# Performance work log

Measured on AMD Instinct MI355X. Metric: run time of the kernel, lower is better.

Reference implementation:

```python
import jax, jax.numpy as jnp
import numpy as np

EMBED_DIM = 1024
NUM_HEADS = 16
MICRO_HEADS = 8
HEAD_DIM = EMBED_DIM // NUM_HEADS
N_BLOCKS = NUM_HEADS // MICRO_HEADS
B, N = 2, 2048


def setup_inputs() -> dict:
    key = jax.random.key(0)
    ks = jax.random.split(key, 9)
    s = 1.0 / np.sqrt(EMBED_DIM)
    return {
        "x": jax.random.normal(ks[0], (B, N, EMBED_DIM), dtype=jnp.float32),
        "Wq": jax.random.uniform(ks[1], (EMBED_DIM, EMBED_DIM), jnp.float32, -s, s),
        "bq": jax.random.uniform(ks[2], (EMBED_DIM,), jnp.float32, -s, s),
        "Wk": jax.random.uniform(ks[3], (EMBED_DIM, EMBED_DIM), jnp.float32, -s, s),
        "bk": jax.random.uniform(ks[4], (EMBED_DIM,), jnp.float32, -s, s),
        "Wv": jax.random.uniform(ks[5], (EMBED_DIM, EMBED_DIM), jnp.float32, -s, s),
        "bv": jax.random.uniform(ks[6], (EMBED_DIM,), jnp.float32, -s, s),
        "Wo": jax.random.uniform(ks[7], (EMBED_DIM, EMBED_DIM), jnp.float32, -s, s),
        "bo": jax.random.uniform(ks[8], (EMBED_DIM,), jnp.float32, -s, s),
    }


def _scramble(t, b, n):
    # Replicates torch's Qh[:, :, hs:he, :].contiguous().view(B*mh, N, dh)
    # which is a raw row-major reshape mixing (N, mh) -> (mh, N) per batch.
    # (B, N, E) -> (B, N, nb, mh, dh) -> (B, nb, N, mh, dh) -> raw reshape -> (B, nb, mh, N, dh)
    t = t.reshape(b, n, N_BLOCKS, MICRO_HEADS, HEAD_DIM)
    t = jnp.transpose(t, (0, 2, 1, 3, 4))
    return t.reshape(b, N_BLOCKS, MICRO_HEADS, n, HEAD_DIM)


def reference(x, Wq, bq, Wk, bk, Wv, bv, Wo, bo):
    b, n, e = x.shape
    scale = HEAD_DIM ** -0.5
    Q = x @ Wq.T + bq
    K = x @ Wk.T + bk
    V = x @ Wv.T + bv
    q = _scramble(Q, b, n)  # (B, nb, mh, N, dh)
    k = _scramble(K, b, n)
    v = _scramble(V, b, n)
    s = jnp.einsum("bgmqd,bgmkd->bgmqk", q, k) * scale  # (B, nb, mh, N, N)
    causal = jnp.tril(jnp.ones((n, n), dtype=bool))
    s = jnp.where(causal, s, -jnp.inf)
    p = jax.nn.softmax(s, axis=-1)
    ctx = jnp.einsum("bgmqk,bgmkd->bgmqd", p, v)  # (B, nb, mh, N, dh)
    # inverse raw reshape: (mh, N, dh) -> (N, mh*dh) per (b, g), then concat blocks
    ctx = ctx.reshape(b, N_BLOCKS, n, MICRO_HEADS * HEAD_DIM)
    ctx = jnp.transpose(ctx, (0, 2, 1, 3)).reshape(b, n, e)
    return ctx @ Wo.T + bo
```

## Files before the change

### kernel.cpp

```cpp
#include <hip/hip_runtime.h>
#include <hip/hip_bf16.h>


typedef unsigned short ushortT;
typedef __attribute__((ext_vector_type(8))) short short8;
typedef __attribute__((ext_vector_type(4))) float floatx4;

__device__ inline float bf2f(ushortT u) {
    union { unsigned int i; float f; } v; v.i = ((unsigned int)u) << 16; return v.f;
}
__device__ inline ushortT f2bf(float f) {
    union { float f; unsigned int i; } v; v.f = f;
    unsigned int x = v.i;
    return (ushortT)((x + 0x7fffu + ((x >> 16) & 1u)) >> 16);
}

__device__ inline void gl_lds16(const ushortT* g, ushortT* lds) {
    __builtin_amdgcn_global_load_lds(
        (const __attribute__((address_space(1))) unsigned int*)g,
        (__attribute__((address_space(3))) unsigned int*)lds, 16, 0, 0);
}

__global__ __launch_bounds__(256) void cvt_bf16(
    const float* __restrict__ x,
    const float* __restrict__ Wq, const float* __restrict__ Wk,
    const float* __restrict__ Wv, const float* __restrict__ Wo,
    ushortT* __restrict__ xb, ushortT* __restrict__ Wb)
{
    const unsigned tid = blockIdx.x * 256 + threadIdx.x;
    const size_t e = (size_t)tid * 8;
    const float* src;
    ushortT* dst;
    size_t off;
    if (e < (size_t)(4u << 20)) { src = x; dst = xb; off = e; }
    else {
        const size_t r = e - (size_t)(4u << 20);
        const int wsel = (int)(r >> 20);
        off = r & 0xFFFFFu;
        src = (wsel == 0) ? Wq : (wsel == 1) ? Wk : (wsel == 2) ? Wv : Wo;
        dst = Wb + ((size_t)wsel << 20);
    }
    const float4 f0 = ((const float4*)(src + off))[0];
    const float4 f1 = ((const float4*)(src + off))[1];
    union { __hip_bfloat162 h[4]; uint4 u; } pk;
    pk.h[0] = __float22bfloat162_rn(float2{f0.x, f0.y});
    pk.h[1] = __float22bfloat162_rn(float2{f0.z, f0.w});
    pk.h[2] = __float22bfloat162_rn(float2{f1.x, f1.y});
    pk.h[3] = __float22bfloat162_rn(float2{f1.z, f1.w});
    *(uint4*)(dst + off) = pk.u;
}

__global__ __launch_bounds__(512, 2) void gemm_qkv_8p(
    const ushortT* __restrict__ A, const ushortT* __restrict__ Wst,
    const float* __restrict__ b0, const float* __restrict__ b1, const float* __restrict__ b2,
    ushortT* __restrict__ O0, ushortT* __restrict__ O1, ushortT* __restrict__ O2)
{
    __shared__ __align__(16) ushortT sm[65536];

    const int t = threadIdx.x;
    const int bid = blockIdx.x;
    const int wg = (bid & 7) * 24 + (bid >> 3);
    const int mt = wg / 12;
    const int nt = wg - mt * 12;
    const int m0 = mt * 256;
    const int mat = nt >> 2;
    const int n0 = (nt & 3) * 256;
    const ushortT* W = Wst + ((size_t)mat << 20);
    const float* bias = (mat == 0) ? b0 : (mat == 1) ? b1 : b2;
    ushortT* Out     = (mat == 0) ? O0 : (mat == 1) ? O1 : O2;

    const int w = t >> 6, lane = t & 63;
    const int wm = w >> 2, wn = w & 3;
    const int col16 = lane & 15, quad = lane >> 4;
    const int c7 = col16 & 7;

    const int ko[2] = { ((0 + quad) ^ c7) << 3, ((4 + quad) ^ c7) << 3 };
    const int xbase = (wm * 128 + col16) * 64;
    const int wbase = (wn * 64 + col16) * 64;

    const int trow = t >> 3;
    const int sch = (t & 7) ^ (trow & 7);
    const ushortT* gA[4]; const ushortT* gB[4];
    #pragma unroll
    for (int q = 0; q < 4; q++) {
        gA[q] = A + (size_t)(m0 + q * 64 + trow) * 1024 + sch * 8;
        gB[q] = W + (size_t)(n0 + q * 64 + trow) * 1024 + sch * 8;
    }
    const int dst0 = (w << 6) * 8;

    floatx4 acc[8][4];
    #pragma unroll
    for (int i = 0; i < 8; i++)
        #pragma unroll
        for (int j = 0; j < 4; j++) acc[i][j] = (floatx4)0.0f;

    auto issue8 = [&](const int ab, const int bb) {
        #pragma unroll
        for (int q = 0; q < 4; q++) {
            gl_lds16(gA[q], sm + ab + dst0 + q * 4096);
            gl_lds16(gB[q], sm + bb + dst0 + q * 4096);
            gA[q] += 64; gB[q] += 64;
        }
    };

    auto group = [&](const int ab, const int bb) {
        short8 bw[4];
        #pragma unroll
        for (int ks = 0; ks < 2; ks++) {
            #pragma unroll
            for (int mh = 0; mh < 2; mh++) {
                short8 bx[4];
                if (mh == 0) {
                    #pragma unroll
                    for (int nf = 0; nf < 4; nf++)
                        bw[nf] = *(const short8*)(sm + bb + wbase + nf * 1024 + ko[ks]);
                }
                #pragma unroll
                for (int j = 0; j < 4; j++)
                    bx[j] = *(const short8*)(sm + ab + xbase + (mh * 4 + j) * 1024 + ko[ks]);
                __builtin_amdgcn_s_barrier();
                __builtin_amdgcn_s_setprio(1);
                #pragma unroll
                for (int j = 0; j < 4; j++)
                    #pragma unroll
                    for (int nf = 0; nf < 4; nf++)
                        acc[mh * 4 + j][nf] = __builtin_amdgcn_mfma_f32_16x16x32_bf16(
                            bw[nf], bx[j], acc[mh * 4 + j][nf], 0, 0, 0);
                __builtin_amdgcn_s_setprio(0);
                __builtin_amdgcn_s_barrier();
            }
        }
    };

    issue8(0, 16384);
    issue8(32768, 49152);

    #pragma unroll 1
    for (int it = 0; it < 7; ++it) {
        asm volatile("s_waitcnt vmcnt(8)" ::: "memory");
        __builtin_amdgcn_s_barrier();
        group(0, 16384);
        issue8(0, 16384);
        asm volatile("s_waitcnt vmcnt(8)" ::: "memory");
        __builtin_amdgcn_s_barrier();
        group(32768, 49152);
        issue8(32768, 49152);
    }
    asm volatile("s_waitcnt vmcnt(8)" ::: "memory");
    __builtin_amdgcn_s_barrier();
    group(0, 16384);
    asm volatile("s_waitcnt vmcnt(0)" ::: "memory");
    __builtin_amdgcn_s_barrier();
    group(32768, 49152);

    #pragma unroll
    for (int mf = 0; mf < 8; mf++) {
        const int m = m0 + wm * 128 + mf * 16 + col16;
        #pragma unroll
        for (int nf = 0; nf < 4; nf++) {
            const int nb = n0 + wn * 64 + nf * 16 + quad * 4;
            const float4 bv4 = *(const float4*)(bias + nb);
            const float v0 = acc[mf][nf][0] + bv4.x;
            const float v1 = acc[mf][nf][1] + bv4.y;
            const float v2 = acc[mf][nf][2] + bv4.z;
            const float v3 = acc[mf][nf][3] + bv4.w;
            union { __hip_bfloat162 h[2]; unsigned long long u; } pk2;
            pk2.h[0] = __float22bfloat162_rn(float2{v0, v1});
            pk2.h[1] = __float22bfloat162_rn(float2{v2, v3});
            *(unsigned long long*)(Out + (size_t)m * 1024 + nb) = pk2.u;
        }
    }
}

template <bool OUT_F32, bool N64>
__global__ __launch_bounds__(256) void gemm_lds(
    const ushortT* __restrict__ A, const ushortT* __restrict__ Wst,
    const float* __restrict__ b0, const float* __restrict__ b1, const float* __restrict__ b2,
    void* __restrict__ O0, void* __restrict__ O1, void* __restrict__ O2)
{
    constexpr int NT = N64 ? 64 : 128;
    constexpr int NJ = N64 ? 2 : 4;
    constexpr int WQ = N64 ? 2 : 4;
    __shared__ __align__(16) ushortT As[128 * 64];
    __shared__ __align__(16) ushortT Bs[NT * 64];
    const int t = threadIdx.x;
    const int m0 = blockIdx.y * 128;
    const int n0g = blockIdx.x * NT;
    const int mat = n0g >> 10;
    const int n0 = n0g & 1023;
    const ushortT* W = Wst + ((size_t)mat << 20);
    const float* bias = (mat == 0) ? b0 : (mat == 1) ? b1 : b2;
    void* Out        = (mat == 0) ? O0 : (mat == 1) ? O1 : O2;

    const int w = t >> 6, lane = t & 63;
    const int wm = w >> 1, wn = w & 1;
    const int col16 = lane & 15, quad = lane >> 4;

    floatx4 acc[4][NJ];
    for (int i = 0; i < 4; i++)
        for (int j = 0; j < NJ; j++) acc[i][j] = (floatx4)0.0f;

    const int cid0 = w * (N64 ? 128 : 256) + lane;

    for (int k0 = 0; k0 < 1024; k0 += 64) {
        #pragma unroll
        for (int q = 0; q < 4; q++) {
            const int cid = w * 256 + q * 64 + lane;
            const int row = cid >> 3;
            const int sch = (cid & 7) ^ (row & 7);
            gl_lds16(A + (size_t)(m0 + row) * 1024 + k0 + sch * 8,
                     As + (size_t)(w * 256 + q * 64) * 8);
        }
        #pragma unroll
        for (int q = 0; q < WQ; q++) {
            const int cid = cid0 + q * 64;
            const int row = cid >> 3;
            const int sch = (cid & 7) ^ (row & 7);
            gl_lds16(W + (size_t)(n0 + row) * 1024 + k0 + sch * 8,
                     Bs + (size_t)(w * (N64 ? 128 : 256) + q * 64) * 8);
        }
        __syncthreads();
        #pragma unroll
        for (int ks = 0; ks < 64; ks += 32) {
            const int cbase = (ks >> 3) + quad;
            const int sw = col16 & 7;
            short8 a[4], b[NJ];
            #pragma unroll
            for (int i = 0; i < 4; i++) {
                const int row = wm * 64 + i * 16 + col16;
                a[i] = *(const short8*)(As + row * 64 + ((cbase ^ sw) << 3));
            }
            #pragma unroll
            for (int j = 0; j < NJ; j++) {
                const int row = wn * (NT / 2) + j * 16 + col16;
                b[j] = *(const short8*)(Bs + row * 64 + ((cbase ^ sw) << 3));
            }
            #pragma unroll
            for (int i = 0; i < 4; i++)
                #pragma unroll
                for (int j = 0; j < NJ; j++)
                    acc[i][j] = __builtin_amdgcn_mfma_f32_16x16x32_bf16(b[j], a[i], acc[i][j], 0, 0, 0);
        }
        __syncthreads();
    }

    #pragma unroll
    for (int i = 0; i < 4; i++) {
        const int m = m0 + wm * 64 + i * 16 + col16;
        #pragma unroll
        for (int j = 0; j < NJ; j++) {
            const int nb = n0 + wn * (NT / 2) + j * 16 + quad * 4;
            const float4 bv4 = *(const float4*)(bias + nb);
            const float v0 = acc[i][j][0] + bv4.x;
            const float v1 = acc[i][j][1] + bv4.y;
            const float v2 = acc[i][j][2] + bv4.z;
            const float v3 = acc[i][j][3] + bv4.w;
            if constexpr (OUT_F32) {
                *(float4*)((float*)Out + (size_t)m * 1024 + nb) = float4{v0, v1, v2, v3};
            } else {
                union { __hip_bfloat162 h[2]; unsigned long long u; } pk2;
                pk2.h[0] = __float22bfloat162_rn(float2{v0, v1});
                pk2.h[1] = __float22bfloat162_rn(float2{v2, v3});
                *(unsigned long long*)((ushortT*)Out + (size_t)m * 1024 + nb) = pk2.u;
            }
        }
    }
}

__global__ __launch_bounds__(256) void transpose_v(
    const ushortT* __restrict__ Vb, ushortT* __restrict__ VT)
{
    __shared__ ushortT L[64 * 65];
    const int bid = blockIdx.x;
    const int pt = bid & 31, s = bid >> 5;
    const int bb = s >> 4, g = (s >> 3) & 1, mh = s & 7;
    const size_t baseoff = (size_t)bb * 2048 * 1024 + (size_t)g * 512;
    const int t = threadIdx.x;
    {
        const int pr = t >> 2, seg = t & 3;
        const int i = mh * 2048 + pt * 64 + pr;
        const uint4* src = (const uint4*)(Vb + baseoff + (size_t)(i >> 3) * 1024 + (i & 7) * 64 + seg * 16);
        union { uint4 u[2]; ushortT h[16]; } tmp;
        tmp.u[0] = src[0]; tmp.u[1] = src[1];
        #pragma unroll
        for (int d = 0; d < 16; d++) L[pr * 65 + seg * 16 + d] = tmp.h[d];
    }
    __syncthreads();
    {
        const int dc = t >> 2, pseg = t & 3;
        union { uint4 u[2]; ushortT h[16]; } tmp;
        #pragma unroll
        for (int j = 0; j < 16; j++) tmp.h[j] = L[(pseg * 16 + j) * 65 + dc];
        uint4* dst = (uint4*)(VT + (size_t)s * 64 * 2048 + (size_t)dc * 2048 + pt * 64 + pseg * 16);
        dst[0] = tmp.u[0]; dst[1] = tmp.u[1];
    }
}

__global__ __launch_bounds__(256) void attn(
    const ushortT* __restrict__ Qb, const ushortT* __restrict__ Kb,
    const ushortT* __restrict__ VT, ushortT* __restrict__ Cb)
{
    __shared__ __align__(16) ushortT lds[20480];

    const int t = threadIdx.x;
    const int bid = blockIdx.x;
    const int xcd = bid & 7;
    const int u = bid >> 3;
    const int s = xcd * 4 + (u & 3);
    const int x5 = u >> 2;
    const int qt = (x5 < 8) ? x5 : (x5 < 16) ? (39 - x5)
                 : (x5 < 24) ? (x5 - 8) : (47 - x5);
    const int bb = s >> 4, g = (s >> 3) & 1, mh = s & 7;

    const int w = t >> 6, lane = t & 63;
    const int col16 = lane & 15, quad = lane >> 4;

    const size_t baseoff = (size_t)bb * 2048 * 1024 + (size_t)g * 512;
    const size_t vtbase  = (size_t)s * 64 * 2048;
    const int i0 = mh * 2048 + qt * 64;
    const int qloc = w * 16 + col16;
    const int c7 = col16 & 7;
    const float KL = 0.125f * 1.44269504f;

    short8 qreg[2];
    {
        const int i = i0 + qloc;
        const ushortT* p = Qb + baseoff + (size_t)(i >> 3) * 1024 + (i & 7) * 64;
        qreg[0] = *(const short8*)(p + quad * 8);
        qreg[1] = *(const short8*)(p + 32 + quad * 8);
    }

    int kbo[2];
    kbo[0] = col16 * 64 + (((0 + quad) ^ c7) << 3);
    kbo[1] = col16 * 64 + (((4 + quad) ^ c7) << 3);
    const int pso0 = 16384 + qloc * 64 + (((0 + quad) ^ c7) << 3);
    const int pso1 = 16384 + qloc * 64 + (((4 + quad) ^ c7) << 3);
    int pwo[4];
    #pragma unroll
    for (int c = 0; c < 4; c++) {
        const int key0 = c * 16 + quad * 4;
        pwo[c] = 16384 + qloc * 64 + ((((key0 >> 3) ^ c7)) << 3) + (key0 & 7);
    }

    const int cid0 = w * 128 + lane, cid1 = cid0 + 64;
    const int row0 = cid0 >> 3, sch0 = (cid0 & 7) ^ (row0 & 7);
    const int row1 = cid1 >> 3, sch1 = (cid1 & 7) ^ (row1 & 7);
    const int jr0 = mh * 2048 + row0;
    const int jr1 = mh * 2048 + row1;
    const ushortT* gk0 = Kb + baseoff + (size_t)(jr0 >> 3) * 1024 + (jr0 & 7) * 64 + sch0 * 8;
    const ushortT* gk1 = Kb + baseoff + (size_t)(jr1 >> 3) * 1024 + (jr1 & 7) * 64 + sch1 * 8;
    const ushortT* gv0 = VT + vtbase + (size_t)row0 * 2048 + sch0 * 8;
    const ushortT* gv1 = VT + vtbase + (size_t)row1 * 2048 + sch1 * 8;
    const int sdK = w * 1024;

    auto stage = [&](int sb) {
        gl_lds16(gk0, lds + sb + sdK);
        gl_lds16(gk1, lds + sb + sdK + 512);
        gl_lds16(gv0, lds + sb + 8192 + sdK);
        gl_lds16(gv1, lds + sb + 8192 + sdK + 512);
        gk0 += 8192; gk1 += 8192; gv0 += 64; gv1 += 64;
    };

    float l_s = 0.f;
    floatx4 Oacc[4];
    for (int c = 0; c < 4; c++) Oacc[c] = (floatx4)0.0f;

    stage(0);
    int sb = 4096;
    for (int kt = 0; kt <= qt; ++kt) {
        __syncthreads();
        if (kt < qt) { stage(sb); sb ^= 4096; }

        floatx4 sc[4];
        for (int c = 0; c < 4; c++) sc[c] = (floatx4)0.0f;
        #pragma unroll
        for (int h = 0; h < 2; h++) {
            const short8 bq = qreg[h];
            #pragma unroll
            for (int c = 0; c < 4; c++) {
                const short8 ak = *(const short8*)(lds + kbo[h] + c * 1024);
                sc[c] = __builtin_amdgcn_mfma_f32_16x16x32_bf16(ak, bq, sc[c], 0, 0, 0);
            }
        }

        if (kt == qt) {
            #pragma unroll
            for (int c = 0; c < 4; c++)
                #pragma unroll
                for (int r = 0; r < 4; r++)
                    if ((c * 16 + quad * 4 + r) > qloc) sc[c][r] = -1e30f;
        }

        float lsum = l_s;
        #pragma unroll
        for (int c = 0; c < 4; c++) {
            #pragma unroll
            for (int r = 0; r < 4; r++) {
                const float pv = exp2f(sc[c][r] * KL);
                sc[c][r] = pv;
                lsum += pv;
            }
            union { __hip_bfloat162 h[2]; unsigned long long u; } pk2;
            pk2.h[0] = __float22bfloat162_rn(float2{sc[c][0], sc[c][1]});
            pk2.h[1] = __float22bfloat162_rn(float2{sc[c][2], sc[c][3]});
            *(unsigned long long*)(lds + pwo[c]) = pk2.u;
        }
        l_s = lsum;

        #pragma unroll
        for (int h = 0; h < 2; h++) {
            const short8 bp = *(const short8*)(lds + (h ? pso1 : pso0));
            #pragma unroll
            for (int c = 0; c < 4; c++) {
                const short8 av = *(const short8*)(lds + kbo[h] + 8192 + c * 1024);
                Oacc[c] = __builtin_amdgcn_mfma_f32_16x16x32_bf16(av, bp, Oacc[c], 0, 0, 0);
            }
        }

        kbo[0] ^= 4096; kbo[1] ^= 4096;
    }

    l_s += __shfl_xor(l_s, 16);
    l_s += __shfl_xor(l_s, 32);

    {
        const int i = i0 + qloc;
        const float inv = 1.0f / l_s;
        ushortT* dst = Cb + baseoff + (size_t)(i >> 3) * 1024 + (i & 7) * 64;
        #pragma unroll
        for (int c = 0; c < 4; c++) {
            union { __hip_bfloat162 h[2]; unsigned long long u; } pk2;
            pk2.h[0] = __float22bfloat162_rn(float2{Oacc[c][0] * inv, Oacc[c][1] * inv});
            pk2.h[1] = __float22bfloat162_rn(float2{Oacc[c][2] * inv, Oacc[c][3] * inv});
            *(unsigned long long*)(dst + c * 16 + quad * 4) = pk2.u;
        }
    }
}

extern "C" void kernel_launch(void* const* d_in, const int* in_sizes, int n_in,
                              void* d_out, int out_size, void* d_ws, size_t ws_size,
                              hipStream_t stream)
{
    const float* x  = (const float*)d_in[0];
    const float* Wq = (const float*)d_in[1];
    const float* bq = (const float*)d_in[2];
    const float* Wk = (const float*)d_in[3];
    const float* bk = (const float*)d_in[4];
    const float* Wv = (const float*)d_in[5];
    const float* bv = (const float*)d_in[6];
    const float* Wo = (const float*)d_in[7];
    const float* bo = (const float*)d_in[8];

    const size_t M1 = (size_t)1024 * 1024;
    ushortT* Wb  = (ushortT*)d_ws;
    ushortT* xb  = Wb + 4 * M1;
    ushortT* Qb  = xb + 4 * M1;
    ushortT* Kb  = Qb + 4 * M1;
    ushortT* Vb  = (ushortT*)d_out;
    ushortT* VTb = xb;
    ushortT* Cb  = Qb;

    dim3 blk(256);
    cvt_bf16<<<dim3(4096), blk, 0, stream>>>(x, Wq, Wk, Wv, Wo, xb, Wb);
    gemm_qkv_8p<<<dim3(192), dim3(512), 0, stream>>>(
        xb, Wb, bq, bk, bv, Qb, Kb, Vb);
    transpose_v<<<dim3(1024), blk, 0, stream>>>(Vb, VTb);
    attn<<<dim3(1024), blk, 0, stream>>>(Qb, Kb, VTb, Cb);
    gemm_lds<true, true><<<dim3(16, 32), blk, 0, stream>>>(
        Cb, Wb + 3 * M1, bo, bo, bo, d_out, d_out, d_out);
}
```

Baseline: 192.7 us.

## Keep attention probabilities in registers via permlane swaps; fold softmax scale into Q

```diff
diff --git a/kernel.cpp b/kernel.cpp
--- a/kernel.cpp
+++ b/kernel.cpp
@@ -5,15 +5,7 @@
 typedef unsigned short ushortT;
 typedef __attribute__((ext_vector_type(8))) short short8;
 typedef __attribute__((ext_vector_type(4))) float floatx4;
-
-__device__ inline float bf2f(ushortT u) {
-    union { unsigned int i; float f; } v; v.i = ((unsigned int)u) << 16; return v.f;
-}
-__device__ inline ushortT f2bf(float f) {
-    union { float f; unsigned int i; } v; v.f = f;
-    unsigned int x = v.i;
-    return (ushortT)((x + 0x7fffu + ((x >> 16) & 1u)) >> 16);
-}
+typedef __attribute__((ext_vector_type(2))) unsigned int uintx2;
 
 __device__ inline void gl_lds16(const ushortT* g, ushortT* lds) {
     __builtin_amdgcn_global_load_lds(
@@ -68,6 +60,7 @@
     const ushortT* W = Wst + ((size_t)mat << 20);
     const float* bias = (mat == 0) ? b0 : (mat == 1) ? b1 : b2;
     ushortT* Out     = (mat == 0) ? O0 : (mat == 1) ? O1 : O2;
+    const float oscale = (mat == 0) ? 0.18033688f : 1.0f;
 
     const int w = t >> 6, lane = t & 63;
     const int wm = w >> 2, wn = w & 3;
@@ -160,10 +153,10 @@
         for (int nf = 0; nf < 4; nf++) {
             const int nb = n0 + wn * 64 + nf * 16 + quad * 4;
             const float4 bv4 = *(const float4*)(bias + nb);
-            const float v0 = acc[mf][nf][0] + bv4.x;
-            const float v1 = acc[mf][nf][1] + bv4.y;
-            const float v2 = acc[mf][nf][2] + bv4.z;
-            const float v3 = acc[mf][nf][3] + bv4.w;
+            const float v0 = (acc[mf][nf][0] + bv4.x) * oscale;
+            const float v1 = (acc[mf][nf][1] + bv4.y) * oscale;
+            const float v2 = (acc[mf][nf][2] + bv4.z) * oscale;
+            const float v3 = (acc[mf][nf][3] + bv4.w) * oscale;
             union { __hip_bfloat162 h[2]; unsigned long long u; } pk2;
             pk2.h[0] = __float22bfloat162_rn(float2{v0, v1});
             pk2.h[1] = __float22bfloat162_rn(float2{v2, v3});
@@ -300,7 +293,7 @@
     const ushortT* __restrict__ Qb, const ushortT* __restrict__ Kb,
     const ushortT* __restrict__ VT, ushortT* __restrict__ Cb)
 {
-    __shared__ __align__(16) ushortT lds[20480];
+    __shared__ __align__(16) ushortT lds[16384];
 
     const int t = threadIdx.x;
     const int bid = blockIdx.x;
@@ -320,7 +313,6 @@
     const int i0 = mh * 2048 + qt * 64;
     const int qloc = w * 16 + col16;
     const int c7 = col16 & 7;
-    const float KL = 0.125f * 1.44269504f;
 
     short8 qreg[2];
     {
@@ -333,14 +325,6 @@
     int kbo[2];
     kbo[0] = col16 * 64 + (((0 + quad) ^ c7) << 3);
     kbo[1] = col16 * 64 + (((4 + quad) ^ c7) << 3);
-    const int pso0 = 16384 + qloc * 64 + (((0 + quad) ^ c7) << 3);
-    const int pso1 = 16384 + qloc * 64 + (((4 + quad) ^ c7) << 3);
-    int pwo[4];
-    #pragma unroll
-    for (int c = 0; c < 4; c++) {
-        const int key0 = c * 16 + quad * 4;
-        pwo[c] = 16384 + qloc * 64 + ((((key0 >> 3) ^ c7)) << 3) + (key0 & 7);
-    }
 
     const int cid0 = w * 128 + lane, cid1 = cid0 + 64;
     const int row0 = cid0 >> 3, sch0 = (cid0 & 7) ^ (row0 & 7);
@@ -361,7 +345,7 @@
         gk0 += 8192; gk1 += 8192; gv0 += 64; gv1 += 64;
     };
 
-    float l_s = 0.f;
+    float l4[4] = {0.f, 0.f, 0.f, 0.f};
     floatx4 Oacc[4];
     for (int c = 0; c < 4; c++) Oacc[c] = (floatx4)0.0f;
 
@@ -391,25 +375,32 @@
                     if ((c * 16 + quad * 4 + r) > qloc) sc[c][r] = -1e30f;
         }
 
-        float lsum = l_s;
+        unsigned pw[4][2];
         #pragma unroll
         for (int c = 0; c < 4; c++) {
-            #pragma unroll
-            for (int r = 0; r < 4; r++) {
-                const float pv = exp2f(sc[c][r] * KL);
-                sc[c][r] = pv;
-                lsum += pv;
-            }
-            union { __hip_bfloat162 h[2]; unsigned long long u; } pk2;
-            pk2.h[0] = __float22bfloat162_rn(float2{sc[c][0], sc[c][1]});
-            pk2.h[1] = __float22bfloat162_rn(float2{sc[c][2], sc[c][3]});
-            *(unsigned long long*)(lds + pwo[c]) = pk2.u;
-        }
-        l_s = lsum;
+            float pv0 = __builtin_amdgcn_exp2f(sc[c][0]);
+            float pv1 = __builtin_amdgcn_exp2f(sc[c][1]);
+            float pv2 = __builtin_amdgcn_exp2f(sc[c][2]);
+            float pv3 = __builtin_amdgcn_exp2f(sc[c][3]);
+            l4[0] += pv0; l4[1] += pv1; l4[2] += pv2; l4[3] += pv3;
+            union { __hip_bfloat162 h; unsigned u; } a, b;
+            a.h = __float22bfloat162_rn(float2{pv0, pv1});
+            b.h = __float22bfloat162_rn(float2{pv2, pv3});
+            pw[c][0] = a.u; pw[c][1] = b.u;
+        }
 
         #pragma unroll
         for (int h = 0; h < 2; h++) {
-            const short8 bp = *(const short8*)(lds + (h ? pso1 : pso0));
+            unsigned dw[4];
+            #pragma unroll
+            for (int uu = 0; uu < 2; uu++) {
+                uintx2 s32 = __builtin_amdgcn_permlane32_swap(pw[2 * h][uu], pw[2 * h + 1][uu], false, false);
+                uintx2 s16 = __builtin_amdgcn_permlane16_swap(s32.x, s32.y, false, false);
+                dw[uu] = s16.x; dw[2 + uu] = s16.y;
+            }
+            union { unsigned u[4]; short8 s; } bpu;
+            bpu.u[0] = dw[0]; bpu.u[1] = dw[1]; bpu.u[2] = dw[2]; bpu.u[3] = dw[3];
+            const short8 bp = bpu.s;
             #pragma unroll
             for (int c = 0; c < 4; c++) {
                 const short8 av = *(const short8*)(lds + kbo[h] + 8192 + c * 1024);
@@ -420,6 +411,7 @@
         kbo[0] ^= 4096; kbo[1] ^= 4096;
     }
 
+    float l_s = (l4[0] + l4[1]) + (l4[2] + l4[3]);
     l_s += __shfl_xor(l_s, 16);
     l_s += __shfl_xor(l_s, 32);
 
```

After: 184.0 us. 1.05x faster.
